# Kernel optimization log

Hardware: AMD Instinct MI355X
Metric: run time of the kernel (lower is better)

Reference implementation:

```python
import jax, jax.numpy as jnp
import numpy as np

B, S, D = 4, 2048, 1024
H = 16
HD = D // H  # 64


def setup_inputs() -> dict:
    key = jax.random.key(0)
    ks = jax.random.split(key, 5)
    std = 1.0 / np.sqrt(D)
    return {
        "x": jax.random.normal(ks[0], (B, S, D), dtype=jnp.float32),
        "Wq": jax.random.normal(ks[1], (D, D), dtype=jnp.float32) * std,
        "Wk": jax.random.normal(ks[2], (D, D), dtype=jnp.float32) * std,
        "Wv": jax.random.normal(ks[3], (D, D), dtype=jnp.float32) * std,
        "Wo": jax.random.normal(ks[4], (D, D), dtype=jnp.float32) * std,
        "bo": jnp.zeros((D,), dtype=jnp.float32),
    }


def reference(x, Wq, Wk, Wv, Wo, bo):
    b, n, d_in = x.shape
    q = (x @ Wq).reshape(b, n, H, HD).transpose(0, 2, 1, 3)  # [b,h,n,hd]
    k = (x @ Wk).reshape(b, n, H, HD).transpose(0, 2, 1, 3)
    v = (x @ Wv).reshape(b, n, H, HD).transpose(0, 2, 1, 3)
    scores = jnp.einsum("bhqd,bhkd->bhqk", q, k)  # full NxN, as in original
    causal = jnp.tril(jnp.ones((n, n), dtype=bool))  # True = keep
    scores = jnp.where(causal, scores, -jnp.inf)
    attn = jax.nn.softmax(scores / np.sqrt(HD), axis=-1)
    # dropout p=0.0 -> identity
    ctx = jnp.einsum("bhqk,bhkd->bqhd", attn, v).reshape(b, n, H * HD)
    return ctx @ Wo + bo
```

## Files before the change

### kernel.cpp

```cpp
#include <hip/hip_runtime.h>
#include <math.h>

#define BATCH 4
#define SLEN 2048
#define DMODEL 1024
#define NH 16
#define HD 64
#define MROWS (BATCH * SLEN)
#define QK_LD 2048

typedef __attribute__((ext_vector_type(8))) short short8;
typedef __attribute__((ext_vector_type(4))) float floatx4;

#define AS1 __attribute__((address_space(1)))
#define AS3 __attribute__((address_space(3)))

__device__ inline unsigned short f2bf(float f) {
    union { float f; unsigned u; } a; a.f = f;
    unsigned r = a.u + 0x7fff + ((a.u >> 16) & 1);
    return (unsigned short)(r >> 16);
}

__device__ inline unsigned pack_bf(float lo, float hi) {
    union { float f; unsigned u; } a, b; a.f = lo; b.f = hi;
    return __builtin_amdgcn_perm(b.u + 0x8000u, a.u + 0x8000u, 0x07060302u);
}
__device__ inline unsigned pack_tr(float lo, float hi) {
    union { float f; unsigned u; } a, b; a.f = lo; b.f = hi;
    return __builtin_amdgcn_perm(b.u, a.u, 0x07060302u);
}

__global__ __launch_bounds__(256) void cvt_all(
    const float* __restrict__ x,
    const float* __restrict__ Wq, const float* __restrict__ Wk,
    const float* __restrict__ Wv, const float* __restrict__ Wo,
    short* __restrict__ xb,
    short* __restrict__ WqkT, short* __restrict__ WvT, short* __restrict__ WoT)
{
    int bid = blockIdx.x;
    if (bid < 8192) {
        int i = (bid * 256 + threadIdx.x) * 4;
        float4 v = *(const float4*)(x + i);
        unsigned short t0 = f2bf(v.x), t1 = f2bf(v.y), t2 = f2bf(v.z), t3 = f2bf(v.w);
        uint2 o;
        o.x = (unsigned)t0 | ((unsigned)t1 << 16);
        o.y = (unsigned)t2 | ((unsigned)t3 << 16);
        *(uint2*)(xb + i) = o;
    } else {
        bid -= 8192;
        int z = bid >> 10;
        int inner = bid & 1023;
        int bxi = inner & 31, byi = inner >> 5;

        const float* W; short* Wt; float sc = 1.0f;
        if (z == 0)      { W = Wq; Wt = WqkT; sc = 0.18033688011112042f; }
        else if (z == 1) { W = Wk; Wt = WqkT + (size_t)DMODEL * DMODEL; }
        else if (z == 2) { W = Wv; Wt = WvT; }
        else             { W = Wo; Wt = WoT; }

        __shared__ float t[32][33];
        int bn = bxi * 32, bk = byi * 32;
        int tx = threadIdx.x & 31, r0 = (threadIdx.x >> 5) * 4;
        #pragma unroll
        for (int i = 0; i < 4; i++)
            t[r0 + i][tx] = W[(size_t)(bk + r0 + i) * DMODEL + bn + tx];
        __syncthreads();
        #pragma unroll
        for (int i = 0; i < 4; i++)
            Wt[(size_t)(bn + r0 + i) * DMODEL + bk + tx] = (short)f2bf(t[tx][r0 + i] * sc);
    }
}

#define TM 128
#define TN 128
#define TK 32

template <int OUT_BF16>
__device__ __forceinline__ void gemm_body(
    const short* __restrict__ A,
    const short* __restrict__ Bt,
    const float* __restrict__ bias,
    void* __restrict__ Cout, int N, int K, int m0, int n0)
{
    __shared__ short As[2][TM * TK];
    __shared__ short Bs[2][TN * TK];
    int tid = threadIdx.x;
    int l = tid & 63, w = tid >> 6;
    int wm = (w >> 1) * 64, wn = (w & 1) * 64;
    int lr = l & 15, lk = (l >> 4) * 8;

    const short* asrc[2];
    const short* bsrc[2];
    #pragma unroll
    for (int r = 0; r < 2; r++) {
        int c = r * 256 + tid;
        int mm = c >> 2, kk = (c & 3) * 8;
        asrc[r] = A  + (size_t)(m0 + mm) * K + kk;
        bsrc[r] = Bt + (size_t)(n0 + mm) * K + kk;
    }

    floatx4 acc[4][4] = {};

    #pragma unroll
    for (int r = 0; r < 2; r++) {
        int c = r * 256 + tid;
        __builtin_amdgcn_global_load_lds((const AS1 void*)asrc[r],
            (AS3 void*)(&As[0][0] + c * 8), 16, 0, 0);
        __builtin_amdgcn_global_load_lds((const AS1 void*)bsrc[r],
            (AS3 void*)(&Bs[0][0] + c * 8), 16, 0, 0);
        asrc[r] += TK; bsrc[r] += TK;
    }

    int nk = K / TK;
    for (int t = 0; t < nk; t++) {
        int cur = t & 1;
        if (t + 1 < nk) {
            #pragma unroll
            for (int r = 0; r < 2; r++) {
                int c = r * 256 + tid;
                __builtin_amdgcn_global_load_lds((const AS1 void*)asrc[r],
                    (AS3 void*)(&As[cur ^ 1][0] + c * 8), 16, 0, 0);
                __builtin_amdgcn_global_load_lds((const AS1 void*)bsrc[r],
                    (AS3 void*)(&Bs[cur ^ 1][0] + c * 8), 16, 0, 0);
                asrc[r] += TK; bsrc[r] += TK;
            }
            asm volatile("s_waitcnt vmcnt(4)" ::: "memory");
        } else {
            asm volatile("s_waitcnt vmcnt(0)" ::: "memory");
        }
        __builtin_amdgcn_s_barrier();
        __builtin_amdgcn_sched_barrier(0);

        short8 af[4], bg[4];
        #pragma unroll
        for (int i = 0; i < 4; i++) {
            af[i] = *(const short8*)(&As[cur][0] + (wm + i * 16 + lr) * TK + lk);
            bg[i] = *(const short8*)(&Bs[cur][0] + (wn + i * 16 + lr) * TK + lk);
        }
        #pragma unroll
        for (int mi = 0; mi < 4; mi++)
            #pragma unroll
            for (int ni = 0; ni < 4; ni++)
                acc[mi][ni] = __builtin_amdgcn_mfma_f32_16x16x32_bf16(
                    af[mi], bg[ni], acc[mi][ni], 0, 0, 0);

        __builtin_amdgcn_sched_barrier(0);
        __builtin_amdgcn_s_barrier();
    }

    int rbase = (l >> 4) * 4, cbase = l & 15;
    if (OUT_BF16) {
        short* C = (short*)Cout;
        #pragma unroll
        for (int mi = 0; mi < 4; mi++)
            #pragma unroll
            for (int r = 0; r < 4; r++) {
                int row = m0 + wm + mi * 16 + rbase + r;
                #pragma unroll
                for (int ni = 0; ni < 4; ni++) {
                    int col = n0 + wn + ni * 16 + cbase;
                    C[(size_t)row * N + col] = (short)f2bf(acc[mi][ni][r]);
                }
            }
    } else {
        float* C = (float*)Cout;
        #pragma unroll
        for (int mi = 0; mi < 4; mi++)
            #pragma unroll
            for (int r = 0; r < 4; r++) {
                int row = m0 + wm + mi * 16 + rbase + r;
                #pragma unroll
                for (int ni = 0; ni < 4; ni++) {
                    int col = n0 + wn + ni * 16 + cbase;
                    C[(size_t)row * N + col] = acc[mi][ni][r] + bias[col];
                }
            }
    }
}

template <int OUT_BF16>
__global__ __launch_bounds__(256) void mfma_gemm(
    const short* __restrict__ A, const short* __restrict__ Bt,
    const float* __restrict__ bias, void* __restrict__ Cout,
    int M, int N, int K)
{
    int m0 = blockIdx.y * TM, n0 = blockIdx.x * TN;
    gemm_body<OUT_BF16>(A, Bt, bias, Cout, N, K, m0, n0);
}

__global__ __launch_bounds__(256) void qkv_gemm(
    const short* __restrict__ xb, const short* __restrict__ WqkT,
    const short* __restrict__ WvT, short* __restrict__ QKb,
    short* __restrict__ VtT)
{
    const short* A; const short* Bt; short* C; int N, m0, n0;
    int bid = blockIdx.x;
    if (bid < 1024) {
        A = xb; Bt = WqkT; C = QKb; N = 2048;
        m0 = (bid >> 4) * TM; n0 = (bid & 15) * TN;
    } else {
        int r = bid - 1024;
        A = WvT; Bt = xb; C = VtT; N = MROWS;
        m0 = (r >> 6) * TM; n0 = (r & 63) * TN;
    }
    gemm_body<1>(A, Bt, nullptr, C, N, DMODEL, m0, n0);
}

#define PSTR 72

__global__ __launch_bounds__(256, 4) void fa_mfma(
    const short* __restrict__ QK, const short* __restrict__ VtT,
    short* __restrict__ ctx)
{
    __shared__ __align__(16) short Ks[2][64][32];
    __shared__ __align__(16) short Vs[2][64][32];
    __shared__ __align__(16) short Ps[4][16][PSTR];

    int tid = threadIdx.x;
    int l = tid & 63, w = tid >> 6;
    int lr = l & 15, lg = l >> 4;
    int bh = blockIdx.x;
    int b = bh >> 4, h = bh & 15;
    int qt = 31 - blockIdx.y;
    int q0 = qt * 64;

    const short* Qbase = QK + (size_t)b * SLEN * QK_LD + h * HD;
    const short* Kbase = Qbase + 1024;
    const short* Vbase = VtT + (size_t)h * HD * MROWS + b * SLEN;

    int xoff = (lg ^ ((lr >> 1) & 3)) * 8;

    short8 ones;
    #pragma unroll
    for (int j = 0; j < 8; j++) ones[j] = (short)0x3F80;

    int qrow = q0 + w * 16 + lr;

    short8 qf[2];
    #pragma unroll
    for (int kk = 0; kk < 2; kk++)
        qf[kk] = *(const short8*)(Qbase + (size_t)qrow * QK_LD + kk * 32 + lg * 8);

    const short* ksrc[2];
    const short* vsrc[2];
    #pragma unroll
    for (int r2 = 0; r2 < 2; r2++) {
        int cc = r2 * 256 + tid;
        int kh = cc >> 8, rr = (cc >> 2) & 63;
        int q = (cc & 3) ^ ((rr >> 1) & 3);
        ksrc[r2] = Kbase + (size_t)rr * QK_LD + kh * 32 + q * 8;
        vsrc[r2] = Vbase + (size_t)rr * MROWS + kh * 32 + q * 8;
    }

    floatx4 O[4] = {};
    floatx4 accL = {};

    for (int kt = 0; kt <= qt; kt++) {
        int k0 = kt * 64;
        __syncthreads();
        #pragma unroll
        for (int r2 = 0; r2 < 2; r2++) {
            int cc = r2 * 256 + tid;
            __builtin_amdgcn_global_load_lds(
                (const AS1 void*)ksrc[r2],
                (AS3 void*)(&Ks[0][0][0] + cc * 8), 16, 0, 0);
            __builtin_amdgcn_global_load_lds(
                (const AS1 void*)vsrc[r2],
                (AS3 void*)(&Vs[0][0][0] + cc * 8), 16, 0, 0);
            ksrc[r2] += (size_t)64 * QK_LD;
            vsrc[r2] += 64;
        }
        __syncthreads();

        floatx4 s4[4] = {};
        #pragma unroll
        for (int kk = 0; kk < 2; kk++)
            #pragma unroll
            for (int t = 0; t < 4; t++) {
                short8 kf = *(const short8*)(&Ks[kk][t * 16 + lr][xoff]);
                s4[t] = __builtin_amdgcn_mfma_f32_16x16x32_bf16(kf, qf[kk], s4[t], 0, 0, 0);
            }

        if (kt == qt) {
            #pragma unroll
            for (int t = 0; t < 4; t++)
                #pragma unroll
                for (int r = 0; r < 4; r++)
                    if (k0 + t * 16 + lg * 4 + r > qrow) s4[t][r] = -INFINITY;
        }

        #pragma unroll
        for (int t = 0; t < 4; t++) {
            float p0 = __builtin_amdgcn_exp2f(s4[t][0]);
            float p1 = __builtin_amdgcn_exp2f(s4[t][1]);
            float p2 = __builtin_amdgcn_exp2f(s4[t][2]);
            float p3 = __builtin_amdgcn_exp2f(s4[t][3]);
            uint2 pk;
            pk.x = pack_tr(p0, p1);
            pk.y = pack_tr(p2, p3);
            *(uint2*)(&Ps[w][lr][t * 16 + lg * 4]) = pk;
        }

        #pragma unroll
        for (int kk = 0; kk < 2; kk++) {
            short8 pf = *(const short8*)(&Ps[w][lr][kk * 32 + lg * 8]);
            accL = __builtin_amdgcn_mfma_f32_16x16x32_bf16(ones, pf, accL, 0, 0, 0);
            #pragma unroll
            for (int dt = 0; dt < 4; dt++) {
                short8 vf = *(const short8*)(&Vs[kk][dt * 16 + lr][xoff]);
                O[dt] = __builtin_amdgcn_mfma_f32_16x16x32_bf16(vf, pf, O[dt], 0, 0, 0);
            }
        }
    }

    float linv = 1.f / accL[0];
    short* crow = ctx + ((size_t)b * SLEN + qrow) * DMODEL + h * HD;
    #pragma unroll
    for (int dt = 0; dt < 4; dt++) {
        uint2 pk;
        pk.x = pack_bf(O[dt][0] * linv, O[dt][1] * linv);
        pk.y = pack_bf(O[dt][2] * linv, O[dt][3] * linv);
        *(uint2*)(crow + dt * 16 + lg * 4) = pk;
    }
}

extern "C" void kernel_launch(void* const* d_in, const int* in_sizes, int n_in,
                              void* d_out, int out_size, void* d_ws, size_t ws_size,
                              hipStream_t stream) {
    const float* x  = (const float*)d_in[0];
    const float* Wq = (const float*)d_in[1];
    const float* Wk = (const float*)d_in[2];
    const float* Wv = (const float*)d_in[3];
    const float* Wo = (const float*)d_in[4];
    const float* bo = (const float*)d_in[5];
    float* out = (float*)d_out;

    const size_t tsz = (size_t)MROWS * DMODEL;
    const size_t wsz = (size_t)DMODEL * DMODEL;

    short* xb    = (short*)d_ws;
    short* WqkT  = xb + tsz;
    short* WvT   = WqkT + 2 * wsz;
    short* WoT   = WvT + wsz;
    short* QKb   = WoT + wsz;
    short* VtT   = QKb + 2 * tsz;
    short* Cb    = VtT + tsz;

    cvt_all<<<12288, 256, 0, stream>>>(x, Wq, Wk, Wv, Wo, xb, WqkT, WvT, WoT);

    qkv_gemm<<<1536, 256, 0, stream>>>(xb, WqkT, WvT, QKb, VtT);

    fa_mfma<<<dim3(BATCH * NH, 32), 256, 0, stream>>>(QKb, VtT, Cb);

    mfma_gemm<0><<<dim3(DMODEL / TN, MROWS / TM), 256, 0, stream>>>(
        Cb, WoT, bo, out, MROWS, DMODEL, DMODEL);
}
```

Baseline: 240.4 us.

## Pair causal query tiles per attention block and loop QKV GEMM tiles per block

The attention kernel now handles two query tiles per block, a long one (31-p) and a short one (p), so every block does about the same amount of causal work and the grid shrinks to 16 in y. The QKV GEMM launches 768 blocks that each process two output tiles in sequence, sharing one LDS buffer passed into gemm_body. Both changes target tail imbalance and block launch overhead. In exchange each block runs longer and there are fewer blocks available to hide latency.

```diff
diff --git a/kernel.cpp b/kernel.cpp
--- a/kernel.cpp
+++ b/kernel.cpp
@@ -80,10 +80,10 @@
     const short* __restrict__ A,
     const short* __restrict__ Bt,
     const float* __restrict__ bias,
-    void* __restrict__ Cout, int N, int K, int m0, int n0)
-{
-    __shared__ short As[2][TM * TK];
-    __shared__ short Bs[2][TN * TK];
+    void* __restrict__ Cout, int N, int K, int m0, int n0, short* smem)
+{
+    short* As = smem;
+    short* Bs = smem + 8192;
     int tid = threadIdx.x;
     int l = tid & 63, w = tid >> 6;
     int wm = (w >> 1) * 64, wn = (w & 1) * 64;
@@ -105,9 +105,9 @@
     for (int r = 0; r < 2; r++) {
         int c = r * 256 + tid;
         __builtin_amdgcn_global_load_lds((const AS1 void*)asrc[r],
-            (AS3 void*)(&As[0][0] + c * 8), 16, 0, 0);
+            (AS3 void*)(As + c * 8), 16, 0, 0);
         __builtin_amdgcn_global_load_lds((const AS1 void*)bsrc[r],
-            (AS3 void*)(&Bs[0][0] + c * 8), 16, 0, 0);
+            (AS3 void*)(Bs + c * 8), 16, 0, 0);
         asrc[r] += TK; bsrc[r] += TK;
     }
 
@@ -119,9 +119,9 @@
             for (int r = 0; r < 2; r++) {
                 int c = r * 256 + tid;
                 __builtin_amdgcn_global_load_lds((const AS1 void*)asrc[r],
-                    (AS3 void*)(&As[cur ^ 1][0] + c * 8), 16, 0, 0);
+                    (AS3 void*)(As + (cur ^ 1) * 4096 + c * 8), 16, 0, 0);
                 __builtin_amdgcn_global_load_lds((const AS1 void*)bsrc[r],
-                    (AS3 void*)(&Bs[cur ^ 1][0] + c * 8), 16, 0, 0);
+                    (AS3 void*)(Bs + (cur ^ 1) * 4096 + c * 8), 16, 0, 0);
                 asrc[r] += TK; bsrc[r] += TK;
             }
             asm volatile("s_waitcnt vmcnt(4)" ::: "memory");
@@ -134,8 +134,8 @@
         short8 af[4], bg[4];
         #pragma unroll
         for (int i = 0; i < 4; i++) {
-            af[i] = *(const short8*)(&As[cur][0] + (wm + i * 16 + lr) * TK + lk);
-            bg[i] = *(const short8*)(&Bs[cur][0] + (wn + i * 16 + lr) * TK + lk);
+            af[i] = *(const short8*)(As + cur * 4096 + (wm + i * 16 + lr) * TK + lk);
+            bg[i] = *(const short8*)(Bs + cur * 4096 + (wn + i * 16 + lr) * TK + lk);
         }
         #pragma unroll
         for (int mi = 0; mi < 4; mi++)
@@ -184,8 +184,9 @@
     const float* __restrict__ bias, void* __restrict__ Cout,
     int M, int N, int K)
 {
-    int m0 = blockIdx.y * TM, n0 = blockIdx.x * TN;
-    gemm_body<OUT_BF16>(A, Bt, bias, Cout, N, K, m0, n0);
+    __shared__ __align__(16) short smem[16384];
+    gemm_body<OUT_BF16>(A, Bt, bias, Cout, N, K,
+                        blockIdx.y * TM, blockIdx.x * TN, smem);
 }
 
 __global__ __launch_bounds__(256) void qkv_gemm(
@@ -193,17 +194,20 @@
     const short* __restrict__ WvT, short* __restrict__ QKb,
     short* __restrict__ VtT)
 {
-    const short* A; const short* Bt; short* C; int N, m0, n0;
+    __shared__ __align__(16) short smem[16384];
     int bid = blockIdx.x;
-    if (bid < 1024) {
-        A = xb; Bt = WqkT; C = QKb; N = 2048;
-        m0 = (bid >> 4) * TM; n0 = (bid & 15) * TN;
-    } else {
-        int r = bid - 1024;
-        A = WvT; Bt = xb; C = VtT; N = MROWS;
-        m0 = (r >> 6) * TM; n0 = (r & 63) * TN;
-    }
-    gemm_body<1>(A, Bt, nullptr, C, N, DMODEL, m0, n0);
+    #pragma unroll 1
+    for (int j = 0; j < 2; j++) {
+        int t = bid + j * 768;
+        if (t < 1024)
+            gemm_body<1>(xb, WqkT, nullptr, QKb, 2048, DMODEL,
+                         (t >> 4) * TM, (t & 15) * TN, smem);
+        else {
+            int r = t - 1024;
+            gemm_body<1>(WvT, xb, nullptr, VtT, MROWS, DMODEL,
+                         (r >> 6) * TM, (r & 63) * TN, smem);
+        }
+    }
 }
 
 #define PSTR 72
@@ -221,8 +225,7 @@
     int lr = l & 15, lg = l >> 4;
     int bh = blockIdx.x;
     int b = bh >> 4, h = bh & 15;
-    int qt = 31 - blockIdx.y;
-    int q0 = qt * 64;
+    int p = blockIdx.y;
 
     const short* Qbase = QK + (size_t)b * SLEN * QK_LD + h * HD;
     const short* Kbase = Qbase + 1024;
@@ -234,93 +237,98 @@
     #pragma unroll
     for (int j = 0; j < 8; j++) ones[j] = (short)0x3F80;
 
-    int qrow = q0 + w * 16 + lr;
-
-    short8 qf[2];
-    #pragma unroll
-    for (int kk = 0; kk < 2; kk++)
-        qf[kk] = *(const short8*)(Qbase + (size_t)qrow * QK_LD + kk * 32 + lg * 8);
-
-    const short* ksrc[2];
-    const short* vsrc[2];
-    #pragma unroll
-    for (int r2 = 0; r2 < 2; r2++) {
-        int cc = r2 * 256 + tid;
-        int kh = cc >> 8, rr = (cc >> 2) & 63;
-        int q = (cc & 3) ^ ((rr >> 1) & 3);
-        ksrc[r2] = Kbase + (size_t)rr * QK_LD + kh * 32 + q * 8;
-        vsrc[r2] = Vbase + (size_t)rr * MROWS + kh * 32 + q * 8;
-    }
-
-    floatx4 O[4] = {};
-    floatx4 accL = {};
-
-    for (int kt = 0; kt <= qt; kt++) {
-        int k0 = kt * 64;
-        __syncthreads();
+    #pragma unroll 1
+    for (int half = 0; half < 2; half++) {
+        int qt = (half == 0) ? (31 - p) : p;
+        int q0 = qt * 64;
+        int qrow = q0 + w * 16 + lr;
+
+        short8 qf[2];
+        #pragma unroll
+        for (int kk = 0; kk < 2; kk++)
+            qf[kk] = *(const short8*)(Qbase + (size_t)qrow * QK_LD + kk * 32 + lg * 8);
+
+        const short* ksrc[2];
+        const short* vsrc[2];
         #pragma unroll
         for (int r2 = 0; r2 < 2; r2++) {
             int cc = r2 * 256 + tid;
-            __builtin_amdgcn_global_load_lds(
-                (const AS1 void*)ksrc[r2],
-                (AS3 void*)(&Ks[0][0][0] + cc * 8), 16, 0, 0);
-            __builtin_amdgcn_global_load_lds(
-                (const AS1 void*)vsrc[r2],
-                (AS3 void*)(&Vs[0][0][0] + cc * 8), 16, 0, 0);
-            ksrc[r2] += (size_t)64 * QK_LD;
-            vsrc[r2] += 64;
-        }
-        __syncthreads();
-
-        floatx4 s4[4] = {};
-        #pragma unroll
-        for (int kk = 0; kk < 2; kk++)
+            int kh = cc >> 8, rr = (cc >> 2) & 63;
+            int q = (cc & 3) ^ ((rr >> 1) & 3);
+            ksrc[r2] = Kbase + (size_t)rr * QK_LD + kh * 32 + q * 8;
+            vsrc[r2] = Vbase + (size_t)rr * MROWS + kh * 32 + q * 8;
+        }
+
+        floatx4 O[4] = {};
+        floatx4 accL = {};
+
+        for (int kt = 0; kt <= qt; kt++) {
+            int k0 = kt * 64;
+            __syncthreads();
+            #pragma unroll
+            for (int r2 = 0; r2 < 2; r2++) {
+                int cc = r2 * 256 + tid;
+                __builtin_amdgcn_global_load_lds(
+                    (const AS1 void*)ksrc[r2],
+                    (AS3 void*)(&Ks[0][0][0] + cc * 8), 16, 0, 0);
+                __builtin_amdgcn_global_load_lds(
+                    (const AS1 void*)vsrc[r2],
+                    (AS3 void*)(&Vs[0][0][0] + cc * 8), 16, 0, 0);
+                ksrc[r2] += (size_t)64 * QK_LD;
+                vsrc[r2] += 64;
+            }
+            __syncthreads();
+
+            floatx4 s4[4] = {};
+            #pragma unroll
+            for (int kk = 0; kk < 2; kk++)
+                #pragma unroll
+                for (int t = 0; t < 4; t++) {
+                    short8 kf = *(const short8*)(&Ks[kk][t * 16 + lr][xoff]);
+                    s4[t] = __builtin_amdgcn_mfma_f32_16x16x32_bf16(kf, qf[kk], s4[t], 0, 0, 0);
+                }
+
+            if (kt == qt) {
+                #pragma unroll
+                for (int t = 0; t < 4; t++)
+                    #pragma unroll
+                    for (int r = 0; r < 4; r++)
+                        if (k0 + t * 16 + lg * 4 + r > qrow) s4[t][r] = -INFINITY;
+            }
+
             #pragma unroll
             for (int t = 0; t < 4; t++) {
-                short8 kf = *(const short8*)(&Ks[kk][t * 16 + lr][xoff]);
-                s4[t] = __builtin_amdgcn_mfma_f32_16x16x32_bf16(kf, qf[kk], s4[t], 0, 0, 0);
-            }
-
-        if (kt == qt) {
-            #pragma unroll
-            for (int t = 0; t < 4; t++)
-                #pragma unroll
-                for (int r = 0; r < 4; r++)
-                    if (k0 + t * 16 + lg * 4 + r > qrow) s4[t][r] = -INFINITY;
-        }
-
-        #pragma unroll
-        for (int t = 0; t < 4; t++) {
-            float p0 = __builtin_amdgcn_exp2f(s4[t][0]);
-            float p1 = __builtin_amdgcn_exp2f(s4[t][1]);
-            float p2 = __builtin_amdgcn_exp2f(s4[t][2]);
-            float p3 = __builtin_amdgcn_exp2f(s4[t][3]);
+                float p0 = __builtin_amdgcn_exp2f(s4[t][0]);
+                float p1 = __builtin_amdgcn_exp2f(s4[t][1]);
+                float p2 = __builtin_amdgcn_exp2f(s4[t][2]);
+                float p3 = __builtin_amdgcn_exp2f(s4[t][3]);
+                uint2 pk;
+                pk.x = pack_tr(p0, p1);
+                pk.y = pack_tr(p2, p3);
+                *(uint2*)(&Ps[w][lr][t * 16 + lg * 4]) = pk;
+            }
+
+            #pragma unroll
+            for (int kk = 0; kk < 2; kk++) {
+                short8 pf = *(const short8*)(&Ps[w][lr][kk * 32 + lg * 8]);
+                accL = __builtin_amdgcn_mfma_f32_16x16x32_bf16(ones, pf, accL, 0, 0, 0);
+                #pragma unroll
+                for (int dt = 0; dt < 4; dt++) {
+                    short8 vf = *(const short8*)(&Vs[kk][dt * 16 + lr][xoff]);
+                    O[dt] = __builtin_amdgcn_mfma_f32_16x16x32_bf16(vf, pf, O[dt], 0, 0, 0);
+                }
+            }
+        }
+
+        float linv = 1.f / accL[0];
+        short* crow = ctx + ((size_t)b * SLEN + qrow) * DMODEL + h * HD;
+        #pragma unroll
+        for (int dt = 0; dt < 4; dt++) {
             uint2 pk;
-            pk.x = pack_tr(p0, p1);
-            pk.y = pack_tr(p2, p3);
-            *(uint2*)(&Ps[w][lr][t * 16 + lg * 4]) = pk;
-        }
-
-        #pragma unroll
-        for (int kk = 0; kk < 2; kk++) {
-            short8 pf = *(const short8*)(&Ps[w][lr][kk * 32 + lg * 8]);
-            accL = __builtin_amdgcn_mfma_f32_16x16x32_bf16(ones, pf, accL, 0, 0, 0);
-            #pragma unroll
-            for (int dt = 0; dt < 4; dt++) {
-                short8 vf = *(const short8*)(&Vs[kk][dt * 16 + lr][xoff]);
-                O[dt] = __builtin_amdgcn_mfma_f32_16x16x32_bf16(vf, pf, O[dt], 0, 0, 0);
-            }
-        }
-    }
-
-    float linv = 1.f / accL[0];
-    short* crow = ctx + ((size_t)b * SLEN + qrow) * DMODEL + h * HD;
-    #pragma unroll
-    for (int dt = 0; dt < 4; dt++) {
-        uint2 pk;
-        pk.x = pack_bf(O[dt][0] * linv, O[dt][1] * linv);
-        pk.y = pack_bf(O[dt][2] * linv, O[dt][3] * linv);
-        *(uint2*)(crow + dt * 16 + lg * 4) = pk;
+            pk.x = pack_bf(O[dt][0] * linv, O[dt][1] * linv);
+            pk.y = pack_bf(O[dt][2] * linv, O[dt][3] * linv);
+            *(uint2*)(crow + dt * 16 + lg * 4) = pk;
+        }
     }
 }
 
@@ -348,9 +356,9 @@
 
     cvt_all<<<12288, 256, 0, stream>>>(x, Wq, Wk, Wv, Wo, xb, WqkT, WvT, WoT);
 
-    qkv_gemm<<<1536, 256, 0, stream>>>(xb, WqkT, WvT, QKb, VtT);
-
-    fa_mfma<<<dim3(BATCH * NH, 32), 256, 0, stream>>>(QKb, VtT, Cb);
+    qkv_gemm<<<768, 256, 0, stream>>>(xb, WqkT, WvT, QKb, VtT);
+
+    fa_mfma<<<dim3(BATCH * NH, 16), 256, 0, stream>>>(QKb, VtT, Cb);
 
     mfma_gemm<0><<<dim3(DMODEL / TN, MROWS / TM), 256, 0, stream>>>(
         Cb, WoT, bo, out, MROWS, DMODEL, DMODEL);
```

Measured after the change: 245.0 us. No clear change (+1.9%).
